# Performance work log

Hardware: AMD Instinct MI355X
Metric: run time of the kernel (lower is better)

## Reference

```python
import jax, jax.numpy as jnp
import numpy as np

BATCH = 1_000_000
NUM_KDE = 500_000
RKHS = 20
OUT = 128
NUM_NODES = 100_000


def setup_inputs() -> dict:
    key = jax.random.key(0)
    ks = jax.random.split(key, 9)
    src = jax.random.randint(ks[0], (BATCH,), 0, NUM_NODES, dtype=jnp.int64 if jax.config.read('jax_enable_x64') else jnp.int32)
    dst = jax.random.randint(ks[1], (BATCH,), 0, NUM_NODES, dtype=src.dtype)
    t_diff = jax.random.uniform(ks[2], (BATCH,), dtype=jnp.float32) * 1000.0
    kde_idx = jax.random.randint(ks[3], (BATCH,), 0, NUM_KDE, dtype=src.dtype)
    kde_mask = jax.random.randint(ks[4], (BATCH,), 0, 2) == 1
    kde_table = jax.random.normal(ks[5], (NUM_KDE, RKHS), dtype=jnp.float32)
    W_proj = jax.random.normal(ks[6], (OUT, RKHS), dtype=jnp.float32) * (1.0 / np.sqrt(RKHS))
    b_proj = jnp.zeros((OUT,), dtype=jnp.float32)
    W_fb = jax.random.normal(ks[7], (OUT, 1), dtype=jnp.float32)
    b_fb = jax.random.normal(ks[8], (OUT,), dtype=jnp.float32)
    return {
        'src': src, 'dst': dst, 't_diff': t_diff,
        'kde_idx': kde_idx, 'kde_mask': kde_mask, 'kde_table': kde_table,
        'W_proj': W_proj, 'b_proj': b_proj, 'W_fb': W_fb, 'b_fb': b_fb,
    }


def reference(src, dst, t_diff, kde_idx, kde_mask, kde_table, W_proj, b_proj, W_fb, b_fb):
    # Gather KDE vectors for every edge (miss rows gather a dummy row, masked out below).
    kde_vecs = kde_table[kde_idx]                       # [B, RKHS]
    # rkhs_projection: Linear(RKHS -> OUT)
    kde_out = jnp.einsum('br,or->bo', kde_vecs, W_proj) + b_proj   # [B, OUT]
    # fallback_encoder: cos(Linear(1 -> OUT))
    fb_out = jnp.cos(t_diff[:, None] * W_fb[:, 0][None, :] + b_fb)  # [B, OUT]
    return jnp.where(kde_mask[:, None], kde_out, fb_out)
```

## Files before the change

### kernel.cpp

```cpp
#include <hip/hip_runtime.h>
#include <hip/hip_bf16.h>

#define BATCH_N 1000000
#define RKHS_N 20
#define OUT_N 128
#define RPW 16
#define WAVES 4
#define ROWS_PER_BLOCK (RPW * WAVES)
#define GRID_N (BATCH_N / ROWS_PER_BLOCK)

__global__ void kde_probe(const unsigned char* __restrict__ mask,
                          const unsigned short* __restrict__ td,
                          unsigned int* __restrict__ cfg)
{
    int i = blockIdx.x * blockDim.x + threadIdx.x;
    unsigned int bits = 0;
    if ((i & 3) != 0 && mask[i] != 0) bits |= 1u;
    if (td[2 * i] & 0x8000u)          bits |= 2u;
    unsigned long long m1 = __ballot(bits & 1u);
    unsigned long long m2 = __ballot(bits & 2u);
    if ((threadIdx.x & 63) == 0) {
        unsigned int v = (m1 ? 1u : 0u) | (m2 ? 2u : 0u);
        if (v) atomicOr(cfg, v);
    }
}

__device__ __forceinline__ float bflo(unsigned int w) {
    return __uint_as_float(w << 16);
}
__device__ __forceinline__ float bfhi(unsigned int w) {
    return __uint_as_float(w & 0xffff0000u);
}

template<bool BF16, bool MASK8>
__device__ __forceinline__ void run_impl(const void* __restrict__ t_diff,
                                         const int* __restrict__ kde_idx,
                                         const void* __restrict__ kde_mask,
                                         const void* __restrict__ kde_table,
                                         const void* __restrict__ W_proj,
                                         const void* __restrict__ b_proj,
                                         const void* __restrict__ W_fb,
                                         const void* __restrict__ b_fb,
                                         void* __restrict__ out,
                                         unsigned int* __restrict__ lds)
{
    constexpr int DW   = BF16 ? 10 : 20;
    constexpr int LDSW = BF16 ? 12 : 20;
    constexpr int TOT  = RPW * DW;

    const int tid  = threadIdx.x;
    const int wave = tid >> 6;
    const int lane = tid & 63;
    const int base = blockIdx.x * ROWS_PER_BLOCK + wave * RPW;

    float w0[RKHS_N], w1[RKHS_N];
    float bp0, bp1, wf0, wf1, bb0, bb1;
    if constexpr (BF16) {
        const unsigned int* wp = (const unsigned int*)W_proj;
#pragma unroll
        for (int d = 0; d < 10; ++d) {
            unsigned int a = wp[lane * 20 + d];
            unsigned int b = wp[lane * 20 + 10 + d];
            w0[2 * d] = bflo(a); w0[2 * d + 1] = bfhi(a);
            w1[2 * d] = bflo(b); w1[2 * d + 1] = bfhi(b);
        }
        unsigned int v;
        v = ((const unsigned int*)b_proj)[lane]; bp0 = bflo(v); bp1 = bfhi(v);
        v = ((const unsigned int*)W_fb)[lane];   wf0 = bflo(v); wf1 = bfhi(v);
        v = ((const unsigned int*)b_fb)[lane];   bb0 = bflo(v); bb1 = bfhi(v);
    } else {
        const float* wp = (const float*)W_proj;
#pragma unroll
        for (int k = 0; k < RKHS_N; ++k) {
            w0[k] = wp[(2 * lane) * RKHS_N + k];
            w1[k] = wp[(2 * lane + 1) * RKHS_N + k];
        }
        bp0 = ((const float*)b_proj)[2 * lane]; bp1 = ((const float*)b_proj)[2 * lane + 1];
        wf0 = ((const float*)W_fb)[2 * lane];   wf1 = ((const float*)W_fb)[2 * lane + 1];
        bb0 = ((const float*)b_fb)[2 * lane];   bb1 = ((const float*)b_fb)[2 * lane + 1];
    }

    unsigned int* wl = lds + wave * (RPW * LDSW);
    const unsigned int* tbl = (const unsigned int*)kde_table;
    constexpr int ITERS = (TOT + 63) / 64;
#pragma unroll
    for (int i = 0; i < ITERS; ++i) {
        int j = lane + 64 * i;
        if ((TOT % 64 == 0) || (j < TOT)) {
            int r = j / DW;
            int d = j - r * DW;
            int idx = kde_idx[base + r];
            wl[r * LDSW + d] = tbl[(size_t)(unsigned)idx * DW + d];
        }
    }

    const unsigned int* mp = (const unsigned int*)kde_mask;
    const unsigned int* tp = (const unsigned int*)t_diff;
#pragma unroll
    for (int r = 0; r < RPW; ++r) {
        unsigned int m;
        if constexpr (MASK8)
            m = (mp[(base >> 2) + (r >> 2)] >> ((r & 3) * 8)) & 0xffu;
        else
            m = mp[base + r];

        float rx, ry;
        if (m) {
            float a0 = bp0, a1 = bp1;
            const unsigned int* rowp = wl + r * LDSW;
            if constexpr (BF16) {
                uint4 q0 = *(const uint4*)(rowp);
                uint4 q1 = *(const uint4*)(rowp + 4);
                uint2 q2 = *(const uint2*)(rowp + 8);
                unsigned int dwv[10] = {q0.x, q0.y, q0.z, q0.w,
                                        q1.x, q1.y, q1.z, q1.w,
                                        q2.x, q2.y};
#pragma unroll
                for (int d = 0; d < 10; ++d) {
                    float v0 = bflo(dwv[d]), v1 = bfhi(dwv[d]);
                    a0 = fmaf(v0, w0[2 * d], a0);
                    a1 = fmaf(v0, w1[2 * d], a1);
                    a0 = fmaf(v1, w0[2 * d + 1], a0);
                    a1 = fmaf(v1, w1[2 * d + 1], a1);
                }
            } else {
                uint4 q[5];
#pragma unroll
                for (int i5 = 0; i5 < 5; ++i5) q[i5] = *(const uint4*)(rowp + 4 * i5);
                const unsigned int* dv = (const unsigned int*)q;
#pragma unroll
                for (int k = 0; k < RKHS_N; ++k) {
                    float v = __uint_as_float(dv[k]);
                    a0 = fmaf(v, w0[k], a0);
                    a1 = fmaf(v, w1[k], a1);
                }
            }
            rx = a0; ry = a1;
        } else {
            float t;
            if constexpr (BF16) {
                unsigned int w = tp[(base >> 1) + (r >> 1)];
                t = (r & 1) ? bfhi(w) : bflo(w);
            } else {
                t = ((const float*)t_diff)[base + r];
            }
            rx = __cosf(fmaf(t, wf0, bb0));
            ry = __cosf(fmaf(t, wf1, bb1));
        }

        size_t g = (size_t)(base + r);
        if constexpr (BF16) {
            __hip_bfloat162 pk;
            pk.x = __float2bfloat16(rx);
            pk.y = __float2bfloat16(ry);
            unsigned int ub;
            __builtin_memcpy(&ub, &pk, 4);
            __builtin_nontemporal_store(ub, (unsigned int*)out + g * 64 + lane);
        } else {
            float2 fv; fv.x = rx; fv.y = ry;
            unsigned long long uv;
            __builtin_memcpy(&uv, &fv, 8);
            __builtin_nontemporal_store(uv, (unsigned long long*)out + g * 64 + lane);
        }
    }
}

__global__ __launch_bounds__(256)
void kde_main(const void* __restrict__ t_diff,
              const int* __restrict__ kde_idx,
              const void* __restrict__ kde_mask,
              const void* __restrict__ kde_table,
              const void* __restrict__ W_proj,
              const void* __restrict__ b_proj,
              const void* __restrict__ W_fb,
              const void* __restrict__ b_fb,
              void* __restrict__ out,
              const unsigned int* __restrict__ cfg)
{
    __shared__ unsigned int lds[WAVES * RPW * 20];
    const unsigned int c = *cfg;
    if (c & 2u) {
        if (c & 1u) run_impl<false, true >(t_diff, kde_idx, kde_mask, kde_table, W_proj, b_proj, W_fb, b_fb, out, lds);
        else        run_impl<false, false>(t_diff, kde_idx, kde_mask, kde_table, W_proj, b_proj, W_fb, b_fb, out, lds);
    } else {
        if (c & 1u) run_impl<true,  true >(t_diff, kde_idx, kde_mask, kde_table, W_proj, b_proj, W_fb, b_fb, out, lds);
        else        run_impl<true,  false>(t_diff, kde_idx, kde_mask, kde_table, W_proj, b_proj, W_fb, b_fb, out, lds);
    }
}

extern "C" void kernel_launch(void* const* d_in, const int* in_sizes, int n_in,
                              void* d_out, int out_size, void* d_ws, size_t ws_size,
                              hipStream_t stream)
{
    const void* t_diff    = d_in[2];
    const int*  kde_idx   = (const int*)d_in[3];
    const void* kde_mask  = d_in[4];
    const void* kde_table = d_in[5];
    const void* W_proj    = d_in[6];
    const void* b_proj    = d_in[7];
    const void* W_fb      = d_in[8];
    const void* b_fb      = d_in[9];

    unsigned int* cfg = (unsigned int*)d_ws;
    hipMemsetAsync(cfg, 0, sizeof(unsigned int), stream);
    kde_probe<<<256, 256, 0, stream>>>((const unsigned char*)kde_mask,
                                       (const unsigned short*)t_diff, cfg);
    kde_main<<<GRID_N, 256, 0, stream>>>(
        t_diff, kde_idx, kde_mask, kde_table, W_proj, b_proj, W_fb, b_fb,
        d_out, cfg);
}
```

Measured before the change: 658.0 us.

## Use persistent grid with double-buffered LDS prefetch of masked table rows

Replaces the one-group-per-wave launch with a fixed persistent grid of 1024 blocks in which each wave loops over 16-row groups. Index, mask and t_diff values for the next two groups are prefetched in registers, and the next group's table rows are loaded during the current group's compute, then written into a second LDS buffer. Table rows are fetched with wider vector chunks and only when the mask marks a dictionary hit, skipping gathers whose results would be discarded. Per-row mask and t values now reach the wave via readlane rather than per-row global loads; the cost is more register pressure and twice the LDS per block.

```diff
diff --git a/kernel.cpp b/kernel.cpp
--- a/kernel.cpp
+++ b/kernel.cpp
@@ -6,8 +6,9 @@
 #define OUT_N 128
 #define RPW 16
 #define WAVES 4
-#define ROWS_PER_BLOCK (RPW * WAVES)
-#define GRID_N (BATCH_N / ROWS_PER_BLOCK)
+#define NBLK 1024
+#define TOTAL_WAVES (NBLK * WAVES)
+#define NGROUPS (BATCH_N / RPW)
 
 __global__ void kde_probe(const unsigned char* __restrict__ mask,
                           const unsigned short* __restrict__ td,
@@ -31,6 +32,17 @@
 __device__ __forceinline__ float bfhi(unsigned int w) {
     return __uint_as_float(w & 0xffff0000u);
 }
+
+template<bool BF16> struct ChunkSel;
+template<> struct ChunkSel<true>  { using T = uint2; };
+template<> struct ChunkSel<false> { using T = uint4; };
+
+struct PFS {
+    int      i0, i1;
+    unsigned m0, m1;
+    unsigned mrow;
+    unsigned trow;
+};
 
 template<bool BF16, bool MASK8>
 __device__ __forceinline__ void run_impl(const void* __restrict__ t_diff,
@@ -44,14 +56,14 @@
                                          void* __restrict__ out,
                                          unsigned int* __restrict__ lds)
 {
-    constexpr int DW   = BF16 ? 10 : 20;
+    constexpr int CH   = BF16 ? 2 : 4;
     constexpr int LDSW = BF16 ? 12 : 20;
-    constexpr int TOT  = RPW * DW;
+    constexpr int WBUF = RPW * LDSW;
+    using CT = typename ChunkSel<BF16>::T;
 
     const int tid  = threadIdx.x;
     const int wave = tid >> 6;
     const int lane = tid & 63;
-    const int base = blockIdx.x * ROWS_PER_BLOCK + wave * RPW;
 
     float w0[RKHS_N], w1[RKHS_N];
     float bp0, bp1, wf0, wf1, bb0, bb1;
@@ -80,88 +92,132 @@
         bb0 = ((const float*)b_fb)[2 * lane];   bb1 = ((const float*)b_fb)[2 * lane + 1];
     }
 
-    unsigned int* wl = lds + wave * (RPW * LDSW);
-    const unsigned int* tbl = (const unsigned int*)kde_table;
-    constexpr int ITERS = (TOT + 63) / 64;
-#pragma unroll
-    for (int i = 0; i < ITERS; ++i) {
-        int j = lane + 64 * i;
-        if ((TOT % 64 == 0) || (j < TOT)) {
-            int r = j / DW;
-            int d = j - r * DW;
-            int idx = kde_idx[base + r];
-            wl[r * LDSW + d] = tbl[(size_t)(unsigned)idx * DW + d];
-        }
-    }
-
-    const unsigned int* mp = (const unsigned int*)kde_mask;
-    const unsigned int* tp = (const unsigned int*)t_diff;
-#pragma unroll
-    for (int r = 0; r < RPW; ++r) {
-        unsigned int m;
-        if constexpr (MASK8)
-            m = (mp[(base >> 2) + (r >> 2)] >> ((r & 3) * 8)) & 0xffu;
-        else
-            m = mp[base + r];
-
-        float rx, ry;
-        if (m) {
-            float a0 = bp0, a1 = bp1;
-            const unsigned int* rowp = wl + r * LDSW;
+    const int  r0  = lane / 5;
+    const int  s0  = lane - 5 * r0;
+    const int  r1  = (lane + 64) / 5;
+    const int  s1  = (lane + 64) - 5 * r1;
+    const bool two = lane < 16;
+
+    const unsigned char*  mb   = (const unsigned char*)kde_mask;
+    const unsigned int*   mp32 = (const unsigned int*)kde_mask;
+    const unsigned short* tp16 = (const unsigned short*)t_diff;
+    const float*          tpf  = (const float*)t_diff;
+    const CT*             tbl  = (const CT*)kde_table;
+
+    auto load_pf = [&](int g) -> PFS {
+        PFS p;
+        const int base = g * RPW;
+        p.i0 = kde_idx[base + r0];
+        p.m0 = MASK8 ? (unsigned)mb[base + r0] : mp32[base + r0];
+        p.i1 = 0; p.m1 = 0; p.mrow = 0; p.trow = 0;
+        if (two) {
+            p.i1 = kde_idx[base + r1];
+            p.m1 = MASK8 ? (unsigned)mb[base + r1] : mp32[base + r1];
+        }
+        if (lane < RPW) {
+            p.mrow = MASK8 ? (unsigned)mb[base + lane] : mp32[base + lane];
+            if constexpr (BF16)
+                p.trow = ((unsigned)tp16[base + lane]) << 16;
+            else
+                p.trow = __float_as_uint(tpf[base + lane]);
+        }
+        return p;
+    };
+
+    auto load_tbl = [&](const PFS& p, CT& d0, CT& d1) {
+        d0 = CT{}; d1 = CT{};
+        if (p.m0)        d0 = tbl[(size_t)(unsigned)p.i0 * 5 + s0];
+        if (two && p.m1) d1 = tbl[(size_t)(unsigned)p.i1 * 5 + s1];
+    };
+
+    auto commit = [&](unsigned int* wl, const PFS& p, const CT& d0, const CT& d1) {
+        if (p.m0)        *(CT*)(wl + r0 * LDSW + s0 * CH) = d0;
+        if (two && p.m1) *(CT*)(wl + r1 * LDSW + s1 * CH) = d1;
+    };
+
+    auto compute = [&](int g, const unsigned int* wl, const PFS& p) {
+        const int base = g * RPW;
+#pragma unroll
+        for (int r = 0; r < RPW; ++r) {
+            unsigned m = (unsigned)__builtin_amdgcn_readlane((int)p.mrow, r);
+            float rx, ry;
+            if (m) {
+                float a0 = bp0, a1 = bp1;
+                const unsigned int* rowp = wl + r * LDSW;
+                if constexpr (BF16) {
+                    uint4 q0 = *(const uint4*)(rowp);
+                    uint4 q1 = *(const uint4*)(rowp + 4);
+                    uint2 q2 = *(const uint2*)(rowp + 8);
+                    unsigned int dwv[10] = {q0.x, q0.y, q0.z, q0.w,
+                                            q1.x, q1.y, q1.z, q1.w,
+                                            q2.x, q2.y};
+#pragma unroll
+                    for (int d = 0; d < 10; ++d) {
+                        float v0 = bflo(dwv[d]), v1 = bfhi(dwv[d]);
+                        a0 = fmaf(v0, w0[2 * d], a0);
+                        a1 = fmaf(v0, w1[2 * d], a1);
+                        a0 = fmaf(v1, w0[2 * d + 1], a0);
+                        a1 = fmaf(v1, w1[2 * d + 1], a1);
+                    }
+                } else {
+                    uint4 q[5];
+#pragma unroll
+                    for (int i5 = 0; i5 < 5; ++i5) q[i5] = *(const uint4*)(rowp + 4 * i5);
+                    const unsigned int* dv = (const unsigned int*)q;
+#pragma unroll
+                    for (int k = 0; k < RKHS_N; ++k) {
+                        float v = __uint_as_float(dv[k]);
+                        a0 = fmaf(v, w0[k], a0);
+                        a1 = fmaf(v, w1[k], a1);
+                    }
+                }
+                rx = a0; ry = a1;
+            } else {
+                float t = __uint_as_float(
+                    (unsigned)__builtin_amdgcn_readlane((int)p.trow, r));
+                rx = __cosf(fmaf(t, wf0, bb0));
+                ry = __cosf(fmaf(t, wf1, bb1));
+            }
+
+            size_t gi = (size_t)(base + r);
             if constexpr (BF16) {
-                uint4 q0 = *(const uint4*)(rowp);
-                uint4 q1 = *(const uint4*)(rowp + 4);
-                uint2 q2 = *(const uint2*)(rowp + 8);
-                unsigned int dwv[10] = {q0.x, q0.y, q0.z, q0.w,
-                                        q1.x, q1.y, q1.z, q1.w,
-                                        q2.x, q2.y};
-#pragma unroll
-                for (int d = 0; d < 10; ++d) {
-                    float v0 = bflo(dwv[d]), v1 = bfhi(dwv[d]);
-                    a0 = fmaf(v0, w0[2 * d], a0);
-                    a1 = fmaf(v0, w1[2 * d], a1);
-                    a0 = fmaf(v1, w0[2 * d + 1], a0);
-                    a1 = fmaf(v1, w1[2 * d + 1], a1);
-                }
+                __hip_bfloat162 pk;
+                pk.x = __float2bfloat16(rx);
+                pk.y = __float2bfloat16(ry);
+                unsigned int ub;
+                __builtin_memcpy(&ub, &pk, 4);
+                __builtin_nontemporal_store(ub, (unsigned int*)out + gi * 64 + lane);
             } else {
-                uint4 q[5];
-#pragma unroll
-                for (int i5 = 0; i5 < 5; ++i5) q[i5] = *(const uint4*)(rowp + 4 * i5);
-                const unsigned int* dv = (const unsigned int*)q;
-#pragma unroll
-                for (int k = 0; k < RKHS_N; ++k) {
-                    float v = __uint_as_float(dv[k]);
-                    a0 = fmaf(v, w0[k], a0);
-                    a1 = fmaf(v, w1[k], a1);
-                }
+                float2 fv; fv.x = rx; fv.y = ry;
+                unsigned long long uv;
+                __builtin_memcpy(&uv, &fv, 8);
+                __builtin_nontemporal_store(uv, (unsigned long long*)out + gi * 64 + lane);
             }
-            rx = a0; ry = a1;
-        } else {
-            float t;
-            if constexpr (BF16) {
-                unsigned int w = tp[(base >> 1) + (r >> 1)];
-                t = (r & 1) ? bfhi(w) : bflo(w);
-            } else {
-                t = ((const float*)t_diff)[base + r];
-            }
-            rx = __cosf(fmaf(t, wf0, bb0));
-            ry = __cosf(fmaf(t, wf1, bb1));
-        }
-
-        size_t g = (size_t)(base + r);
-        if constexpr (BF16) {
-            __hip_bfloat162 pk;
-            pk.x = __float2bfloat16(rx);
-            pk.y = __float2bfloat16(ry);
-            unsigned int ub;
-            __builtin_memcpy(&ub, &pk, 4);
-            __builtin_nontemporal_store(ub, (unsigned int*)out + g * 64 + lane);
-        } else {
-            float2 fv; fv.x = rx; fv.y = ry;
-            unsigned long long uv;
-            __builtin_memcpy(&uv, &fv, 8);
-            __builtin_nontemporal_store(uv, (unsigned long long*)out + g * 64 + lane);
-        }
+        }
+    };
+
+    unsigned int* wl0 = lds + wave * (2 * WBUF);
+    unsigned int* wl1 = wl0 + WBUF;
+
+    int g = blockIdx.x * WAVES + wave;
+    PFS cur = load_pf(g);
+    CT d0, d1;
+    load_tbl(cur, d0, d1);
+    commit(wl0, cur, d0, d1);
+    int gn = g + TOTAL_WAVES;
+    PFS nxt{};
+    if (gn < NGROUPS) nxt = load_pf(gn);
+    int cb = 0;
+    for (;;) {
+        const bool have = (gn < NGROUPS);
+        if (have) load_tbl(nxt, d0, d1);
+        const int gnn = gn + TOTAL_WAVES;
+        PFS n2{};
+        if (gnn < NGROUPS) n2 = load_pf(gnn);
+        compute(g, cb ? wl1 : wl0, cur);
+        if (!have) break;
+        commit(cb ? wl0 : wl1, nxt, d0, d1);
+        cur = nxt; nxt = n2; g = gn; gn = gnn; cb ^= 1;
     }
 }
 
@@ -177,7 +233,7 @@
               void* __restrict__ out,
               const unsigned int* __restrict__ cfg)
 {
-    __shared__ unsigned int lds[WAVES * RPW * 20];
+    __shared__ unsigned int lds[WAVES * 2 * RPW * 20];
     const unsigned int c = *cfg;
     if (c & 2u) {
         if (c & 1u) run_impl<false, true >(t_diff, kde_idx, kde_mask, kde_table, W_proj, b_proj, W_fb, b_fb, out, lds);
@@ -205,7 +261,7 @@
     hipMemsetAsync(cfg, 0, sizeof(unsigned int), stream);
     kde_probe<<<256, 256, 0, stream>>>((const unsigned char*)kde_mask,
                                        (const unsigned short*)t_diff, cfg);
-    kde_main<<<GRID_N, 256, 0, stream>>>(
+    kde_main<<<NBLK, 256, 0, stream>>>(
         t_diff, kde_idx, kde_mask, kde_table, W_proj, b_proj, W_fb, b_fb,
         d_out, cfg);
 }
```

New measurement: 588.3 us. 1.12x faster.
